# Kernel optimization log

Measured on AMD Instinct MI355X. Metric: run time of the kernel, lower is better.

## Reference

```python
import jax, jax.numpy as jnp
import numpy as np

E = 8        # n_experts
K = 2        # top-k
DIM = 1024
HID = 2048   # swiglu hidden; fc1 out = 2*HID
B, T = 4, 2048


def setup_inputs() -> dict:
    key = jax.random.key(0)
    ks = jax.random.split(key, 7)
    s = 0.02
    return {
        "x": jax.random.normal(ks[0], (B, T, DIM), dtype=jnp.float32),
        "router_w": jax.random.normal(ks[1], (E, DIM), dtype=jnp.float32) * s,
        "router_b": jnp.zeros((E,), dtype=jnp.float32),
        "W1": jax.random.normal(ks[2], (E, DIM, 2 * HID), dtype=jnp.float32) * s,
        "b1": jnp.zeros((E, 2 * HID), dtype=jnp.float32),
        "W2": jax.random.normal(ks[3], (E, HID, DIM), dtype=jnp.float32) * s,
        "b2": jnp.zeros((E, DIM), dtype=jnp.float32),
    }


def _swiglu(h):
    h1, h2 = jnp.split(h, 2, axis=-1)
    return jax.nn.silu(h1) * h2


def reference(x, router_w, router_b, W1, b1, W2, b2):
    # Router: logits = Linear(dim, E), temperature = 1.0
    logits = jnp.einsum("btd,ed->bte", x, router_w) + router_b  # [B,T,E]
    topk_val, topk_idx = jax.lax.top_k(logits, K)               # [B,T,K]
    weights = jax.nn.softmax(topk_val, axis=-1)                 # softmax router
    # combine[b,t,e] = sum_k weights[b,t,k] * [topk_idx[b,t,k] == e]
    combine = jnp.sum(jax.nn.one_hot(topk_idx, E, dtype=x.dtype)
                      * weights[..., None], axis=-2)            # [B,T,E]
    out = jnp.zeros_like(x)
    # Fixed small loop over experts (structurally distinct weight slices).
    for e in range(E):
        h = jnp.einsum("btd,dh->bth", x, W1[e]) + b1[e]         # [B,T,2H]
        y = jnp.einsum("bth,hd->btd", _swiglu(h), W2[e]) + b2[e]
        out = out + combine[..., e:e + 1] * y
    return out
```

## Files before the change

kernel.cpp:

```cpp
#include <hip/hip_runtime.h>
#include <stdint.h>

typedef unsigned short u16;

#define E_    8
#define DIM_  1024
#define HID_  2048
#define H2_   4096
#define NTOK  8192
#define RTOK  32
#define NT1   16
#define NT2   32

typedef __attribute__((ext_vector_type(8))) short bf16x8;
typedef __attribute__((ext_vector_type(4))) float f32x4;
typedef __attribute__((ext_vector_type(4))) unsigned int u32x4;

__device__ __forceinline__ u16 f2bf(float f) {
  uint32_t u = __builtin_bit_cast(uint32_t, f);
  uint32_t r = (u + 0x7FFFu + ((u >> 16) & 1u)) >> 16;
  return (u16)r;
}
__device__ __forceinline__ float bf2f(u16 u) {
  return __builtin_bit_cast(float, (uint32_t)u << 16);
}

__device__ __forceinline__ void gload16(const void* g, void* l) {
  __builtin_amdgcn_global_load_lds(
      (const __attribute__((address_space(1))) void*)g,
      (__attribute__((address_space(3))) void*)l, 16, 0, 0);
}

__device__ __forceinline__ uint32_t lds_addr(const void* p) {
  return (uint32_t)(uintptr_t)(const __attribute__((address_space(3))) void*)p;
}
__device__ __forceinline__ bf16x8 ldsr(uint32_t a) {
  u32x4 r;
  asm volatile("ds_read_b128 %0, %1" : "=v"(r) : "v"(a));
  return __builtin_bit_cast(bf16x8, r);
}

#define MFMA_ __builtin_amdgcn_mfma_f32_16x16x32_bf16
#define SB0   __builtin_amdgcn_sched_barrier(0)


__global__ void cvt_x(const float* __restrict__ x, u16* __restrict__ xb, int n8) {
  int i = blockIdx.x * blockDim.x + threadIdx.x;
  if (i >= n8) return;
  const float4* p = (const float4*)(x + (size_t)i * 8);
  float4 a = p[0], b = p[1];
  union { u16 u[8]; uint4 v; } r;
  r.u[0] = f2bf(a.x); r.u[1] = f2bf(a.y); r.u[2] = f2bf(a.z); r.u[3] = f2bf(a.w);
  r.u[4] = f2bf(b.x); r.u[5] = f2bf(b.y); r.u[6] = f2bf(b.z); r.u[7] = f2bf(b.w);
  *(uint4*)(xb + (size_t)i * 8) = r.v;
}

__global__ void tconv(const float* __restrict__ src, u16* __restrict__ dst, int R, int C) {
  __shared__ float t[64][65];
  int e = blockIdx.z;
  int r0 = blockIdx.y * 64, c0 = blockIdx.x * 64;
  const float* s = src + (size_t)e * R * C;
  u16* d = dst + (size_t)e * R * C;
  int tid = threadIdx.x;
  int rr = tid >> 4, cc = (tid & 15) * 4;
#pragma unroll
  for (int p = 0; p < 4; ++p) {
    float4 v = *(const float4*)(s + (size_t)(r0 + p * 16 + rr) * C + c0 + cc);
    t[p * 16 + rr][cc + 0] = v.x; t[p * 16 + rr][cc + 1] = v.y;
    t[p * 16 + rr][cc + 2] = v.z; t[p * 16 + rr][cc + 3] = v.w;
  }
  __syncthreads();
  int cr = tid >> 3, rc = (tid & 7) * 8;
#pragma unroll
  for (int p = 0; p < 2; ++p) {
    union { u16 u[8]; uint4 v; } w;
#pragma unroll
    for (int j = 0; j < 8; ++j) w.u[j] = f2bf(t[rc + j][p * 32 + cr]);
    *(uint4*)(d + (size_t)(c0 + p * 32 + cr) * R + r0 + rc) = w.v;
  }
}


__global__ void router(const float* __restrict__ x, const float* __restrict__ rw,
                       const float* __restrict__ rb, int* __restrict__ counts,
                       int* __restrict__ btok, float* __restrict__ bw,
                       int* __restrict__ tokrec) {
  __shared__ float srw[E_ * DIM_];
  __shared__ float sb[E_];
  __shared__ int   hcnt[E_], hbase[E_];
  __shared__ int   te[RTOK * 2];
  __shared__ float twt[RTOK * 2];
  __shared__ int   tloc[RTOK * 2];

  int tid = threadIdx.x;
  for (int i = tid; i < E_ * DIM_ / 4; i += 256)
    ((float4*)srw)[i] = ((const float4*)rw)[i];
  if (tid < E_) { sb[tid] = rb[tid]; hcnt[tid] = 0; }
  __syncthreads();

  int wid = tid >> 6, lane = tid & 63;
#pragma unroll
  for (int s = 0; s < RTOK / 4; ++s) {
    int lt = wid * (RTOK / 4) + s;
    int t = blockIdx.x * RTOK + lt;
    const float* xt = x + (size_t)t * DIM_;
    float acc[8] = {0.f, 0.f, 0.f, 0.f, 0.f, 0.f, 0.f, 0.f};
#pragma unroll
    for (int it = 0; it < 4; ++it) {
      int d = it * 256 + lane * 4;
      float4 xv = *(const float4*)(xt + d);
#pragma unroll
      for (int e = 0; e < 8; ++e) {
        float4 rv = *(const float4*)(&srw[e * DIM_ + d]);
        acc[e] += xv.x * rv.x + xv.y * rv.y + xv.z * rv.z + xv.w * rv.w;
      }
    }
#pragma unroll
    for (int e = 0; e < 8; ++e)
#pragma unroll
      for (int off = 32; off; off >>= 1)
        acc[e] += __shfl_xor(acc[e], off, 64);
    if (lane == 0) {
      float v[8];
#pragma unroll
      for (int e = 0; e < 8; ++e) v[e] = acc[e] + sb[e];
      int i0 = 0;
#pragma unroll
      for (int e = 1; e < 8; ++e) if (v[e] > v[i0]) i0 = e;
      int i1 = (i0 == 0) ? 1 : 0;
#pragma unroll
      for (int e = 0; e < 8; ++e) if (e != i0 && v[e] > v[i1]) i1 = e;
      float w0 = 1.f / (1.f + expf(v[i1] - v[i0]));
      float w1 = 1.f - w0;
      int l0 = atomicAdd(&hcnt[i0], 1);
      int l1 = atomicAdd(&hcnt[i1], 1);
      te[lt * 2 + 0] = i0; twt[lt * 2 + 0] = w0; tloc[lt * 2 + 0] = l0;
      te[lt * 2 + 1] = i1; twt[lt * 2 + 1] = w1; tloc[lt * 2 + 1] = l1;
    }
  }
  __syncthreads();
  if (tid < E_) hbase[tid] = atomicAdd(&counts[tid], hcnt[tid]);
  __syncthreads();
  if (tid < RTOK * 2) {
    int e = te[tid];
    int p = hbase[e] + tloc[tid];
    int t = blockIdx.x * RTOK + (tid >> 1);
    btok[e * NTOK + p] = t;
    bw[e * NTOK + p] = twt[tid];
    tokrec[t * 2 + (tid & 1)] = (e << 13) | p;
  }
}


#define STG2(sm_, pArr, buf, reg, half, tile, NTt)                         \
  {                                                                        \
    int tc_ = (tile) < (NTt) ? (tile) : (NTt)-1;                           \
    u16* d_ = (sm_) + (buf)*32768 + (reg)*16384 + (half)*8192 + wid * 512; \
    gload16(pArr[(half)*2 + 0] + tc_ * 64, d_);                            \
    gload16(pArr[(half)*2 + 1] + tc_ * 64, d_ + 4096);                     \
  }

template <int NTt>
__device__ __forceinline__ void kloop(u16* __restrict__ sm,
                                      const u16* const* pA, const u16* const* pB,
                                      int wid, int wr, int wc, int l15, int lhi,
                                      int rxor, f32x4 (&acc)[8][4]) {
  STG2(sm, pA, 0, 0, 0, 0, NTt); STG2(sm, pA, 0, 0, 1, 0, NTt);
  STG2(sm, pB, 0, 1, 0, 0, NTt); STG2(sm, pB, 0, 1, 1, 0, NTt);
  asm volatile("s_waitcnt vmcnt(0)" ::: "memory");
  __builtin_amdgcn_s_barrier();

  const uint32_t k0 = (uint32_t)(((lhi * 8) ^ rxor) * 2);
  const uint32_t k1 = (uint32_t)((((4 + lhi) * 8) ^ rxor) * 2);
  const uint32_t base = lds_addr(sm);

  for (int t = 0; t < NTt; ++t) {
    int cur = t & 1, nb = (t + 1) & 1;
    uint32_t aB = base + (uint32_t)(cur * 65536) + (uint32_t)((wr * 128 + l15) * 128);
    uint32_t bB = base + (uint32_t)(cur * 65536 + 32768) + (uint32_t)((wc * 64 + l15) * 128);

    bf16x8 b[4][2];
#pragma unroll
    for (int n = 0; n < 4; ++n) {
      b[n][0] = ldsr(bB + (uint32_t)(n * 2048) + k0);
      b[n][1] = ldsr(bB + (uint32_t)(n * 2048) + k1);
    }

#pragma unroll
    for (int q = 0; q < 4; ++q) {
      bf16x8 a[2][2];
#pragma unroll
      for (int m = 0; m < 2; ++m) {
        a[m][0] = ldsr(aB + (uint32_t)((q * 2 + m) * 2048) + k0);
        a[m][1] = ldsr(aB + (uint32_t)((q * 2 + m) * 2048) + k1);
      }
      if (q == 0)      STG2(sm, pB, nb, 1, 0, t + 1, NTt)
      else if (q == 1) STG2(sm, pB, nb, 1, 1, t + 1, NTt)
      else if (q == 2) STG2(sm, pA, nb, 0, 0, t + 1, NTt)
      else             STG2(sm, pA, nb, 0, 1, t + 1, NTt)
      asm volatile("s_waitcnt lgkmcnt(0)");
      SB0;
      __builtin_amdgcn_s_setprio(1);
#pragma unroll
      for (int m = 0; m < 2; ++m)
#pragma unroll
        for (int n = 0; n < 4; ++n) {
          acc[q * 2 + m][n] = MFMA_(a[m][0], b[n][0], acc[q * 2 + m][n], 0, 0, 0);
          acc[q * 2 + m][n] = MFMA_(a[m][1], b[n][1], acc[q * 2 + m][n], 0, 0, 0);
        }
      __builtin_amdgcn_s_setprio(0);
    }
    asm volatile("s_waitcnt vmcnt(0)" ::: "memory");
    __builtin_amdgcn_s_barrier();
  }
}


__launch_bounds__(512, 2)
__global__ void gemm1(const u16* __restrict__ xb, const u16* __restrict__ w1t,
                      const float* __restrict__ b1, const int* __restrict__ counts,
                      const int* __restrict__ btok, u16* __restrict__ hb) {
  int e = blockIdx.z, mblk = blockIdx.y, nblk = blockIdx.x;
  int cnt = counts[e];
  if (mblk * 256 >= cnt) return;
  int base = 0;
#pragma unroll
  for (int i = 0; i < 8; ++i) base += (i < e) ? counts[i] : 0;

  __shared__ u16 sm[65536];
  __shared__ int sTok[256];

  int tid = threadIdx.x, wid = tid >> 6, lane = tid & 63;
  if (tid < 256) {
    int gr = mblk * 256 + tid;
    sTok[tid] = (gr < cnt) ? btok[e * NTOK + gr] : btok[e * NTOK];
  }
  __syncthreads();

  int wr = wid >> 2, wc = wid & 3;
  int l15 = lane & 15, lhi = lane >> 4;
  int rxor = (l15 & 7) * 8;
  int segsw = ((tid & 7) ^ ((tid >> 3) & 7)) * 8;
  int rowi = tid >> 3;

  const u16* pA[4];
  const u16* pB[4];
  const size_t w1e = (size_t)e * H2_ * DIM_;
#pragma unroll
  for (int j = 0; j < 4; ++j) {
    int r = j * 64 + rowi;
    pA[j] = xb + (size_t)sTok[r] * DIM_ + segsw;
    int gcol = nblk * 128 + j * 32 + (rowi & 31) + ((rowi >> 5) & 1) * 2048;
    pB[j] = w1t + w1e + (size_t)gcol * DIM_ + segsw;
  }

  f32x4 acc[8][4] = {};
  kloop<NT1>(sm, pA, pB, wid, wr, wc, l15, lhi, rxor, acc);

#pragma unroll
  for (int q = 0; q < 2; ++q) {
    int oc = nblk * 128 + wc * 32 + q * 16 + l15;
    float bb1 = b1[e * H2_ + oc];
    float bb2 = b1[e * H2_ + oc + HID_];
#pragma unroll
    for (int m = 0; m < 8; ++m) {
#pragma unroll
      for (int j = 0; j < 4; ++j) {
        int rt = wr * 128 + m * 16 + lhi * 4 + j;
        int gr = mblk * 256 + rt;
        if (gr < cnt) {
          float h1 = acc[m][q][j] + bb1;
          float h2 = acc[m][q + 2][j] + bb2;
          float s = (h1 / (1.f + __expf(-h1))) * h2;
          hb[(size_t)(base + gr) * HID_ + oc] = f2bf(s);
        }
      }
    }
  }
}


__launch_bounds__(512, 2)
__global__ void gemm2(const u16* __restrict__ hb, const u16* __restrict__ w2t,
                      const float* __restrict__ b2, const int* __restrict__ counts,
                      const float* __restrict__ bw, u16* __restrict__ ybuf) {
  int e = blockIdx.z, mblk = blockIdx.y, nblk = blockIdx.x;
  int cnt = counts[e];
  if (mblk * 256 >= cnt) return;
  int base = 0;
#pragma unroll
  for (int i = 0; i < 8; ++i) base += (i < e) ? counts[i] : 0;

  __shared__ u16 sm[65536];
  __shared__ float sW[256];

  int tid = threadIdx.x, wid = tid >> 6, lane = tid & 63;
  if (tid < 256) {
    int gr = mblk * 256 + tid;
    sW[tid] = (gr < cnt) ? bw[e * NTOK + gr] : 0.f;
  }
  __syncthreads();

  int wr = wid >> 2, wc = wid & 3;
  int l15 = lane & 15, lhi = lane >> 4;
  int rxor = (l15 & 7) * 8;
  int segsw = ((tid & 7) ^ ((tid >> 3) & 7)) * 8;
  int rowi = tid >> 3;

  const u16* pA[4];
  const u16* pB[4];
#pragma unroll
  for (int j = 0; j < 4; ++j) {
    pA[j] = hb + (size_t)(base + mblk * 256 + j * 64 + rowi) * HID_ + segsw;
    pB[j] = w2t + (size_t)e * DIM_ * HID_ +
            (size_t)(nblk * 256 + j * 64 + rowi) * HID_ + segsw;
  }

  f32x4 acc[8][4] = {};
  kloop<NT2>(sm, pA, pB, wid, wr, wc, l15, lhi, rxor, acc);

#pragma unroll
  for (int q = 0; q < 4; ++q) {
    int col = nblk * 256 + wc * 64 + q * 16 + l15;
    float bb = b2[e * DIM_ + col];
#pragma unroll
    for (int m = 0; m < 8; ++m) {
#pragma unroll
      for (int j = 0; j < 4; ++j) {
        int rt = wr * 128 + m * 16 + lhi * 4 + j;
        int gr = mblk * 256 + rt;
        if (gr < cnt)
          ybuf[(size_t)(base + gr) * DIM_ + col] = f2bf(sW[rt] * (acc[m][q][j] + bb));
      }
    }
  }
}


__global__ void combine(const u16* __restrict__ ybuf, const int* __restrict__ tokrec,
                        const int* __restrict__ counts, float* __restrict__ out) {
  __shared__ int sbase[8];
  int tid = threadIdx.x;
  if (tid == 0) {
    int b = 0;
#pragma unroll
    for (int e = 0; e < 8; ++e) { sbase[e] = b; b += counts[e]; }
  }
  __syncthreads();
  int t = blockIdx.x;
  int r0 = tokrec[t * 2 + 0], r1 = tokrec[t * 2 + 1];
  size_t s0 = (size_t)(sbase[r0 >> 13] + (r0 & 8191)) * DIM_;
  size_t s1 = (size_t)(sbase[r1 >> 13] + (r1 & 8191)) * DIM_;
  int c = tid * 4;
  ushort4 a = *(const ushort4*)(ybuf + s0 + c);
  ushort4 b = *(const ushort4*)(ybuf + s1 + c);
  float4 o;
  o.x = bf2f(a.x) + bf2f(b.x);
  o.y = bf2f(a.y) + bf2f(b.y);
  o.z = bf2f(a.z) + bf2f(b.z);
  o.w = bf2f(a.w) + bf2f(b.w);
  *(float4*)(out + (size_t)t * DIM_ + c) = o;
}


extern "C" void kernel_launch(void* const* d_in, const int* in_sizes, int n_in,
                              void* d_out, int out_size, void* d_ws, size_t ws_size,
                              hipStream_t stream) {
  const float* x  = (const float*)d_in[0];
  const float* rw = (const float*)d_in[1];
  const float* rb = (const float*)d_in[2];
  const float* W1 = (const float*)d_in[3];
  const float* b1 = (const float*)d_in[4];
  const float* W2 = (const float*)d_in[5];
  const float* b2 = (const float*)d_in[6];
  float* out = (float*)d_out;

  char* ws = (char*)d_ws;
  int*   counts = (int*)ws;
  int*   btok   = (int*)(ws + 256);
  float* bw     = (float*)(ws + 256 + 262144);
  int*   tokrec = (int*)(ws + 256 + 524288);
  u16* xb  = (u16*)(ws + (1u << 20));
  u16* w1t = xb  + (size_t)NTOK * DIM_;
  u16* w2t = w1t + (size_t)E_ * H2_ * DIM_;
  u16* hb  = w2t + (size_t)E_ * DIM_ * HID_;
  u16* ybuf = w1t;

  hipMemsetAsync(counts, 0, 8 * sizeof(int), stream);

  cvt_x<<<(NTOK * DIM_ / 8 + 255) / 256, 256, 0, stream>>>(x, xb, NTOK * DIM_ / 8);
  tconv<<<dim3(H2_ / 64, DIM_ / 64, E_), 256, 0, stream>>>(W1, w1t, DIM_, H2_);
  tconv<<<dim3(DIM_ / 64, HID_ / 64, E_), 256, 0, stream>>>(W2, w2t, HID_, DIM_);
  router<<<NTOK / RTOK, 256, 0, stream>>>(x, rw, rb, counts, btok, bw, tokrec);

  gemm1<<<dim3(H2_ / 256, NTOK / 256, E_), 512, 0, stream>>>(xb, w1t, b1, counts, btok, hb);
  gemm2<<<dim3(DIM_ / 256, NTOK / 256, E_), 512, 0, stream>>>(hb, w2t, b2, counts, bw, ybuf);
  combine<<<NTOK, 256, 0, stream>>>(ybuf, tokrec, counts, out);
}
```

Baseline: 447.9 us.

## Restructure GEMM k-loop into half-K stages with deeper prefetch and new swizzle

The shared GEMM main loop now splits each 64-wide K tile into two 32-wide halves, each stored in its own LDS region with a new 4-way XOR swizzle. Global-to-LDS loads run up to two stages ahead, and vmcnt(8) waits replace full drains, so memory latency can overlap with MFMA work. MFMA issue is reorganised into 8x2 blocks that reuse the A fragments, with extra barriers between B sub-stages. The added barriers and the tighter reuse of buffers raise the risk of stalls or races if the wait counts do not match the number of loads in flight.

```diff
diff --git a/kernel.cpp b/kernel.cpp
--- a/kernel.cpp
+++ b/kernel.cpp
@@ -152,67 +152,83 @@
 }
 
 
-#define STG2(sm_, pArr, buf, reg, half, tile, NTt)                         \
-  {                                                                        \
-    int tc_ = (tile) < (NTt) ? (tile) : (NTt)-1;                           \
-    u16* d_ = (sm_) + (buf)*32768 + (reg)*16384 + (half)*8192 + wid * 512; \
-    gload16(pArr[(half)*2 + 0] + tc_ * 64, d_);                            \
-    gload16(pArr[(half)*2 + 1] + tc_ * 64, d_ + 4096);                     \
-  }
+#define STGA(bb, kh, tt, NTt)                                               \
+  { int tc_ = (tt) < (NTt) ? (tt) : (NTt) - 1;                              \
+    gload16(pA[0] + tc_ * 64 + (kh) * 32,                                   \
+            sm + (bb) * 32768 + (kh) * 8192 + tid * 8);                     \
+    gload16(pA[1] + tc_ * 64 + (kh) * 32,                                   \
+            sm + (bb) * 32768 + (kh) * 8192 + 4096 + tid * 8); }
+#define STGB(bb, kh, tt, NTt)                                               \
+  { int tc_ = (tt) < (NTt) ? (tt) : (NTt) - 1;                              \
+    gload16(pB[0] + tc_ * 64 + (kh) * 32,                                   \
+            sm + (bb) * 32768 + 16384 + (kh) * 8192 + tid * 8);             \
+    gload16(pB[1] + tc_ * 64 + (kh) * 32,                                   \
+            sm + (bb) * 32768 + 16384 + (kh) * 8192 + 4096 + tid * 8); }
+#define FENCE asm volatile("" ::: "memory")
 
 template <int NTt>
 __device__ __forceinline__ void kloop(u16* __restrict__ sm,
                                       const u16* const* pA, const u16* const* pB,
-                                      int wid, int wr, int wc, int l15, int lhi,
-                                      int rxor, f32x4 (&acc)[8][4]) {
-  STG2(sm, pA, 0, 0, 0, 0, NTt); STG2(sm, pA, 0, 0, 1, 0, NTt);
-  STG2(sm, pB, 0, 1, 0, 0, NTt); STG2(sm, pB, 0, 1, 1, 0, NTt);
-  asm volatile("s_waitcnt vmcnt(0)" ::: "memory");
+                                      int tid, int wr, int wc, int l15, int lhi,
+                                      f32x4 (&acc)[8][4]) {
+  STGA(0, 0, 0, NTt); STGB(0, 0, 0, NTt);
+  STGA(0, 1, 0, NTt); STGB(0, 1, 0, NTt);
+  STGA(1, 0, 1, NTt); STGB(1, 0, 1, NTt);
+  asm volatile("s_waitcnt vmcnt(8)" ::: "memory");
   __builtin_amdgcn_s_barrier();
 
-  const uint32_t k0 = (uint32_t)(((lhi * 8) ^ rxor) * 2);
-  const uint32_t k1 = (uint32_t)((((4 + lhi) * 8) ^ rxor) * 2);
+  const uint32_t fo = (uint32_t)(((lhi ^ l15 ^ (l15 >> 2)) & 3) * 16);
   const uint32_t base = lds_addr(sm);
+  const uint32_t arow = (uint32_t)((wr * 128 + l15) * 64);
+  const uint32_t brow = (uint32_t)((wc * 64 + l15) * 64);
 
   for (int t = 0; t < NTt; ++t) {
-    int cur = t & 1, nb = (t + 1) & 1;
-    uint32_t aB = base + (uint32_t)(cur * 65536) + (uint32_t)((wr * 128 + l15) * 128);
-    uint32_t bB = base + (uint32_t)(cur * 65536 + 32768) + (uint32_t)((wc * 64 + l15) * 128);
-
-    bf16x8 b[4][2];
-#pragma unroll
-    for (int n = 0; n < 4; ++n) {
-      b[n][0] = ldsr(bB + (uint32_t)(n * 2048) + k0);
-      b[n][1] = ldsr(bB + (uint32_t)(n * 2048) + k1);
-    }
-
-#pragma unroll
-    for (int q = 0; q < 4; ++q) {
-      bf16x8 a[2][2];
-#pragma unroll
-      for (int m = 0; m < 2; ++m) {
-        a[m][0] = ldsr(aB + (uint32_t)((q * 2 + m) * 2048) + k0);
-        a[m][1] = ldsr(aB + (uint32_t)((q * 2 + m) * 2048) + k1);
-      }
-      if (q == 0)      STG2(sm, pB, nb, 1, 0, t + 1, NTt)
-      else if (q == 1) STG2(sm, pB, nb, 1, 1, t + 1, NTt)
-      else if (q == 2) STG2(sm, pA, nb, 0, 0, t + 1, NTt)
-      else             STG2(sm, pA, nb, 0, 1, t + 1, NTt)
+    int c = t & 1, o = c ^ 1;
+    bf16x8 a[8];
+#pragma unroll
+    for (int ks = 0; ks < 2; ++ks) {
+      uint32_t aR = base + (uint32_t)(c * 65536 + ks * 16384) + arow + fo;
+      uint32_t bR = base + (uint32_t)(c * 65536 + 32768 + ks * 16384) + brow + fo;
+
+      bf16x8 b0 = ldsr(bR);
+      bf16x8 b1 = ldsr(bR + 1024);
+#pragma unroll
+      for (int m = 0; m < 8; ++m) a[m] = ldsr(aR + (uint32_t)(m * 1024));
+      if (ks == 0) STGA(o, 1, t + 1, NTt)
+      else         STGA(c, 0, t + 2, NTt)
+      FENCE;
+      __builtin_amdgcn_s_barrier();
       asm volatile("s_waitcnt lgkmcnt(0)");
       SB0;
       __builtin_amdgcn_s_setprio(1);
 #pragma unroll
-      for (int m = 0; m < 2; ++m)
-#pragma unroll
-        for (int n = 0; n < 4; ++n) {
-          acc[q * 2 + m][n] = MFMA_(a[m][0], b[n][0], acc[q * 2 + m][n], 0, 0, 0);
-          acc[q * 2 + m][n] = MFMA_(a[m][1], b[n][1], acc[q * 2 + m][n], 0, 0, 0);
-        }
+      for (int m = 0; m < 8; ++m) {
+        acc[m][0] = MFMA_(a[m], b0, acc[m][0], 0, 0, 0);
+        acc[m][1] = MFMA_(a[m], b1, acc[m][1], 0, 0, 0);
+      }
       __builtin_amdgcn_s_setprio(0);
+      __builtin_amdgcn_s_barrier();
+
+      bf16x8 b2 = ldsr(bR + 2048);
+      bf16x8 b3 = ldsr(bR + 3072);
+      if (ks == 0) STGB(o, 1, t + 1, NTt)
+      else         STGB(c, 0, t + 2, NTt)
+      FENCE;
+      __builtin_amdgcn_s_barrier();
+      asm volatile("s_waitcnt lgkmcnt(0)");
+      SB0;
+      __builtin_amdgcn_s_setprio(1);
+#pragma unroll
+      for (int m = 0; m < 8; ++m) {
+        acc[m][2] = MFMA_(a[m], b2, acc[m][2], 0, 0, 0);
+        acc[m][3] = MFMA_(a[m], b3, acc[m][3], 0, 0, 0);
+      }
+      __builtin_amdgcn_s_setprio(0);
+      asm volatile("s_waitcnt vmcnt(8)" ::: "memory");
+      __builtin_amdgcn_s_barrier();
     }
-    asm volatile("s_waitcnt vmcnt(0)" ::: "memory");
-    __builtin_amdgcn_s_barrier();
-  }
+  }
+  asm volatile("s_waitcnt vmcnt(0)" ::: "memory");
 }
 
 
@@ -239,23 +255,23 @@
 
   int wr = wid >> 2, wc = wid & 3;
   int l15 = lane & 15, lhi = lane >> 4;
-  int rxor = (l15 & 7) * 8;
-  int segsw = ((tid & 7) ^ ((tid >> 3) & 7)) * 8;
-  int rowi = tid >> 3;
-
-  const u16* pA[4];
-  const u16* pB[4];
+  int sw = (((tid & 3) ^ ((tid >> 2) & 3) ^ ((tid >> 4) & 3)) & 3) * 8;
+  int r0 = tid >> 2, r1 = r0 + 128;
+
+  const u16* pA[2];
+  const u16* pB[2];
   const size_t w1e = (size_t)e * H2_ * DIM_;
-#pragma unroll
-  for (int j = 0; j < 4; ++j) {
-    int r = j * 64 + rowi;
-    pA[j] = xb + (size_t)sTok[r] * DIM_ + segsw;
-    int gcol = nblk * 128 + j * 32 + (rowi & 31) + ((rowi >> 5) & 1) * 2048;
-    pB[j] = w1t + w1e + (size_t)gcol * DIM_ + segsw;
+  pA[0] = xb + (size_t)sTok[r0] * DIM_ + sw;
+  pA[1] = xb + (size_t)sTok[r1] * DIM_ + sw;
+  {
+    int g0 = nblk * 128 + (r0 >> 6) * 32 + (r0 & 31) + ((r0 >> 5) & 1) * 2048;
+    int g1 = nblk * 128 + (r1 >> 6) * 32 + (r1 & 31) + ((r1 >> 5) & 1) * 2048;
+    pB[0] = w1t + w1e + (size_t)g0 * DIM_ + sw;
+    pB[1] = w1t + w1e + (size_t)g1 * DIM_ + sw;
   }
 
   f32x4 acc[8][4] = {};
-  kloop<NT1>(sm, pA, pB, wid, wr, wc, l15, lhi, rxor, acc);
+  kloop<NT1>(sm, pA, pB, tid, wr, wc, l15, lhi, acc);
 
 #pragma unroll
   for (int q = 0; q < 2; ++q) {
@@ -303,21 +319,18 @@
 
   int wr = wid >> 2, wc = wid & 3;
   int l15 = lane & 15, lhi = lane >> 4;
-  int rxor = (l15 & 7) * 8;
-  int segsw = ((tid & 7) ^ ((tid >> 3) & 7)) * 8;
-  int rowi = tid >> 3;
-
-  const u16* pA[4];
-  const u16* pB[4];
-#pragma unroll
-  for (int j = 0; j < 4; ++j) {
-    pA[j] = hb + (size_t)(base + mblk * 256 + j * 64 + rowi) * HID_ + segsw;
-    pB[j] = w2t + (size_t)e * DIM_ * HID_ +
-            (size_t)(nblk * 256 + j * 64 + rowi) * HID_ + segsw;
-  }
+  int sw = (((tid & 3) ^ ((tid >> 2) & 3) ^ ((tid >> 4) & 3)) & 3) * 8;
+  int r0 = tid >> 2, r1 = r0 + 128;
+
+  const u16* pA[2];
+  const u16* pB[2];
+  pA[0] = hb + (size_t)(base + mblk * 256 + r0) * HID_ + sw;
+  pA[1] = hb + (size_t)(base + mblk * 256 + r1) * HID_ + sw;
+  pB[0] = w2t + (size_t)e * DIM_ * HID_ + (size_t)(nblk * 256 + r0) * HID_ + sw;
+  pB[1] = w2t + (size_t)e * DIM_ * HID_ + (size_t)(nblk * 256 + r1) * HID_ + sw;
 
   f32x4 acc[8][4] = {};
-  kloop<NT2>(sm, pA, pB, wid, wr, wc, l15, lhi, rxor, acc);
+  kloop<NT2>(sm, pA, pB, tid, wr, wc, l15, lhi, acc);
 
 #pragma unroll
   for (int q = 0; q < 4; ++q) {
```

Result: no change. 454.4 us (+1.5%).
